# Kernel optimization log

Measured on AMD Instinct MI355X. Metric: run time of the kernel, lower is better.

The kernel has to match this reference:

```python
import jax, jax.numpy as jnp
import numpy as np

EPS = 1e-6                                   # VN leaky-relu denominator eps
BN_SCALE = np.float32(1.0 / np.sqrt(1.0 + 1e-5))  # eval-mode BatchNorm with default stats
NEG = 0.2                                    # negative_slope


def vn_lin(x, w):
    # x: [n, c, 3, ...]; w: [c, o] -> [n, o, 3, ...]
    return jnp.einsum('nc...,co->no...', x, w)


def vn_act(p, d):
    # Vector-Neuron leaky ReLU: project p off the half-space defined by direction d.
    dot = jnp.sum(p * d, axis=2, keepdims=True)
    dsq = jnp.sum(d * d, axis=2, keepdims=True)
    corr = p - (dot / (dsq + EPS)) * d
    return NEG * p + (1.0 - NEG) * jnp.where(dot >= 0, p, corr)


def score_net(x, w_vn, wd_vn, w_h1, w_h2, b_h2, temp=1.0):
    # CorrelationNet: VNLinearLeakyReLU(3 -> 2*ks) -> norm -> 1x1 convs -> softmax
    p = vn_lin(x, w_vn) * BN_SCALE           # [N, 2ks, 3, K] (VNBatchNorm ~ scalar in eval)
    d = vn_lin(x, wd_vn)
    s = vn_act(p, d)
    s = jnp.linalg.norm(s, axis=2)           # [N, 2ks, K]
    s = jax.nn.relu(jnp.einsum('nck,co->nok', s, w_h1) * BN_SCALE)  # conv1d k=1, BN, relu
    s = jnp.einsum('nck,co->nok', s, w_h2) + b_h2[None, :, None]     # last conv with bias
    return jax.nn.softmax(s / temp, axis=1)  # [N, ks, K]


def setup_inputs() -> dict:
    key = jax.random.key(0)
    k = [jax.random.fold_in(key, i) for i in range(13)]
    N, N2, K, KS, OUT = 16000, 20000, 16, 8, 64
    half = OUT // 2
    return {
        'q_pts': jax.random.normal(k[0], (N, 3), jnp.float32),
        's_pts': jax.random.normal(k[1], (N2, 3), jnp.float32),
        's_feats': jax.random.normal(k[2], (N2, 1, 3), jnp.float32),
        'neighbor_indices': jax.random.randint(k[3], (N, K), 0, N2),
        'wb': jax.random.normal(k[4], (3, KS * half), jnp.float32) * np.float32(np.sqrt(2.0 / 3.0)),
        'w_vn': jax.random.normal(k[5], (3, 2 * KS), jnp.float32) * 0.5,
        'wd_vn': jax.random.normal(k[6], (3, 2 * KS), jnp.float32) * 0.5,
        'w_h1': jax.random.normal(k[7], (2 * KS, KS), jnp.float32) * 0.25,
        'w_h2': jax.random.normal(k[8], (KS, KS), jnp.float32) * 0.35,
        'b_h2': jnp.zeros((KS,), jnp.float32),
        'wd_relu': jax.random.normal(k[9], (half, half), jnp.float32) * 0.18,
        'w_un': jax.random.normal(k[10], (half, OUT), jnp.float32) * 0.18,
        'wd_un': jax.random.normal(k[11], (half, OUT), jnp.float32) * 0.18,
    }


def reference(q_pts, s_pts, s_feats, neighbor_indices, wb, w_vn, wd_vn,
              w_h1, w_h2, b_h2, wd_relu, w_un, wd_un):
    N, K = neighbor_indices.shape
    KS = w_h2.shape[1]
    # neighbor gather + centering: [N, K, 3] -> [N, 1, 3, K]
    pts = s_pts[neighbor_indices] - q_pts[:, None]
    pts = jnp.transpose(pts, (0, 2, 1))[:, None]
    centers = jnp.broadcast_to(jnp.mean(pts, axis=-1, keepdims=True), pts.shape)
    cross = jnp.cross(pts, centers, axis=2)
    local = jnp.concatenate([pts, centers, cross], axis=1)   # [N, 3, 3, K]
    scores = score_net(local, w_vn, wd_vn, w_h1, w_h2, b_h2)  # [N, KS, K]
    # kernel-point correlation conv
    pro = jnp.einsum('ncdk,cf->nfdk', local, wb)              # [N, KS*half, 3, K]
    pro = pro.reshape(N, KS, -1, 3, K)
    pro = jnp.sum(pro * scores[:, :, None, None, :], axis=1)  # [N, half, 3, K]
    nrm = jnp.linalg.norm(pro, axis=2, keepdims=True)
    normed = pro / jnp.maximum(nrm, 1e-12)                    # F.normalize(p=2, dim=2)
    feats = jnp.mean(normed, axis=-1)                         # [N, half, 3]
    feats = vn_act(feats, vn_lin(feats, wd_relu))             # VNLeakyReLU
    out = vn_act(vn_lin(feats, w_un) * BN_SCALE, vn_lin(feats, wd_un))  # VNLinearLeakyReLU
    return out                                                # [N, out_dim, 3]
```

## Files before the change

### kernel.cpp

```cpp
#include <hip/hip_runtime.h>
#include <math.h>

#define VN_EPS   1e-6f
#define NEG      0.2f
#define POS      0.8f

typedef float v2f __attribute__((ext_vector_type(2)));
typedef float v4f __attribute__((ext_vector_type(4)));

template <int CTRL>
__device__ __forceinline__ float dpp_add(float v) {
    int s = __builtin_amdgcn_update_dpp(0, __float_as_int(v), CTRL, 0xf, 0xf, true);
    return v + __int_as_float(s);
}
__device__ __forceinline__ float row16_allsum(float v) {
    v = dpp_add<0x128>(v);
    v = dpp_add<0x124>(v);
    v = dpp_add<0x122>(v);
    v = dpp_add<0x121>(v);
    return v;
}
__device__ __forceinline__ float row16_sum15(float v) {
    v = dpp_add<0x118>(v);
    v = dpp_add<0x114>(v);
    v = dpp_add<0x112>(v);
    v = dpp_add<0x111>(v);
    return v;
}

__global__ __launch_bounds__(128) void areconv_kernel(
    const float* __restrict__ q_pts,
    const float* __restrict__ s_pts,
    const int*   __restrict__ nbr,
    const float* __restrict__ wb,
    const float* __restrict__ w_vn,
    const float* __restrict__ wd_vn,
    const float* __restrict__ w_h1,
    const float* __restrict__ w_h2,
    const float* __restrict__ b_h2,
    const float* __restrict__ wd_relu,
    const float* __restrict__ w_un,
    const float* __restrict__ wd_un,
    float* __restrict__ out,
    int N)
{
    const float BN_SCALE = 0.999994993f;

    __shared__ __align__(16) float featsA [8][3][36];
    __shared__ __align__(16) float feats2A[8][3][36];

    const int tid  = threadIdx.x;
    const int wv   = tid >> 6;
    const int lane = tid & 63;
    const int p    = lane >> 4;
    const int k    = lane & 15;
    const int bp   = wv * 4 + p;
    int n = blockIdx.x * 8 + bp;
    n = (n < N) ? n : (N - 1);

    const float qx = q_pts[n * 3 + 0];
    const float qy = q_pts[n * 3 + 1];
    const float qz = q_pts[n * 3 + 2];
    const int   id = nbr[n * 16 + k];
    const float px = s_pts[id * 3 + 0] - qx;
    const float py = s_pts[id * 3 + 1] - qy;
    const float pz = s_pts[id * 3 + 2] - qz;

    const float cx = row16_allsum(px) * 0.0625f;
    const float cy = row16_allsum(py) * 0.0625f;
    const float cz = row16_allsum(pz) * 0.0625f;

    const float rx = py * cz - pz * cy;
    const float ry = pz * cx - px * cz;
    const float rz = px * cy - py * cx;

    const float L[3][3] = {{px, py, pz}, {cx, cy, cz}, {rx, ry, rz}};

    v2f t01 = {0.f, 0.f}, t23 = t01, t45 = t01, t67 = t01;
#pragma unroll 1
    for (int o = 0; o < 16; ++o) {
        const float wv0 = w_vn[o],  wv1 = w_vn[16 + o],  wv2 = w_vn[32 + o];
        const float wd0 = wd_vn[o], wd1 = wd_vn[16 + o], wd2 = wd_vn[32 + o];
        float pv[3], dv[3];
        float dot = 0.f, dsq = 0.f;
#pragma unroll
        for (int d = 0; d < 3; ++d) {
            const float pp = BN_SCALE * (L[0][d] * wv0 + L[1][d] * wv1 + L[2][d] * wv2);
            const float dd = L[0][d] * wd0 + L[1][d] * wd1 + L[2][d] * wd2;
            pv[d] = pp; dv[d] = dd;
            dot += pp * dd;
            dsq += dd * dd;
        }
        const float f = dot * __builtin_amdgcn_rcpf(dsq + VN_EPS);
        float acc = 0.f;
#pragma unroll
        for (int d = 0; d < 3; ++d) {
            const float corr = pv[d] - f * dv[d];
            const float sel  = (dot >= 0.f) ? pv[d] : corr;
            const float a    = NEG * pv[d] + POS * sel;
            acc += a * a;
        }
        const float s = __builtin_amdgcn_sqrtf(acc);
        t01 += s * (*(const v2f*)&w_h1[o * 8 + 0]);
        t23 += s * (*(const v2f*)&w_h1[o * 8 + 2]);
        t45 += s * (*(const v2f*)&w_h1[o * 8 + 4]);
        t67 += s * (*(const v2f*)&w_h1[o * 8 + 6]);
    }
    float tt[8];
    tt[0] = fmaxf(t01[0] * BN_SCALE, 0.f);  tt[1] = fmaxf(t01[1] * BN_SCALE, 0.f);
    tt[2] = fmaxf(t23[0] * BN_SCALE, 0.f);  tt[3] = fmaxf(t23[1] * BN_SCALE, 0.f);
    tt[4] = fmaxf(t45[0] * BN_SCALE, 0.f);  tt[5] = fmaxf(t45[1] * BN_SCALE, 0.f);
    tt[6] = fmaxf(t67[0] * BN_SCALE, 0.f);  tt[7] = fmaxf(t67[1] * BN_SCALE, 0.f);

    float sc[8];
    float mx = -1e30f;
#pragma unroll
    for (int op = 0; op < 4; ++op) {
        v2f u = *(const v2f*)&b_h2[2 * op];
#pragma unroll
        for (int c = 0; c < 8; ++c)
            u += tt[c] * (*(const v2f*)&w_h2[c * 8 + 2 * op]);
        sc[2 * op + 0] = u[0];
        sc[2 * op + 1] = u[1];
        mx = fmaxf(mx, fmaxf(u[0], u[1]));
    }
    float se = 0.f;
#pragma unroll
    for (int o = 0; o < 8; ++o) { sc[o] = __expf(sc[o] - mx); se += sc[o]; }
    const float inv_se = __builtin_amdgcn_rcpf(se);
#pragma unroll
    for (int o = 0; o < 8; ++o) sc[o] *= inv_se;

#pragma unroll 1
    for (int grp = 0; grp < 8; ++grp) {
        const int hb = grp * 4;
        v4f W0 = sc[0] * (*(const v4f*)&wb[0 * 256 + hb]);
        v4f W1 = sc[0] * (*(const v4f*)&wb[1 * 256 + hb]);
        v4f W2 = sc[0] * (*(const v4f*)&wb[2 * 256 + hb]);
#pragma unroll
        for (int s = 1; s < 8; ++s) {
            const float sv = sc[s];
            W0 += sv * (*(const v4f*)&wb[0 * 256 + s * 32 + hb]);
            W1 += sv * (*(const v4f*)&wb[1 * 256 + s * 32 + hb]);
            W2 += sv * (*(const v4f*)&wb[2 * 256 + s * 32 + hb]);
        }
        v4f V0 = L[0][0] * W0 + L[1][0] * W1 + L[2][0] * W2;
        v4f V1 = L[0][1] * W0 + L[1][1] * W1 + L[2][1] * W2;
        v4f V2 = L[0][2] * W0 + L[1][2] * W1 + L[2][2] * W2;
        v4f vv = V0 * V0 + V1 * V1 + V2 * V2;
        v4f inn;
#pragma unroll
        for (int e = 0; e < 4; ++e)
            inn[e] = __builtin_amdgcn_rsqf(fmaxf(vv[e], 1e-24f)) * 0.0625f;
        V0 *= inn; V1 *= inn; V2 *= inn;
        v4f X0, X1, X2;
#pragma unroll
        for (int e = 0; e < 4; ++e) {
            X0[e] = row16_sum15(V0[e]);
            X1[e] = row16_sum15(V1[e]);
            X2[e] = row16_sum15(V2[e]);
        }
        if (k == 15) {
            *(v4f*)&featsA[bp][0][hb] = X0;
            *(v4f*)&featsA[bp][1][hb] = X1;
            *(v4f*)&featsA[bp][2][hb] = X2;
        }
    }

    {
        v2f D0 = {0.f, 0.f}, D1 = D0, D2 = D0;
#pragma unroll 1
        for (int grp = 0; grp < 8; ++grp) {
            const int hb = grp * 4;
            const v4f f0 = *(const v4f*)&featsA[bp][0][hb];
            const v4f f1 = *(const v4f*)&featsA[bp][1][hb];
            const v4f f2 = *(const v4f*)&featsA[bp][2][hb];
#pragma unroll
            for (int e = 0; e < 4; ++e) {
                const v2f w = *(const v2f*)&wd_relu[(hb + e) * 32 + 2 * k];
                D0 += f0[e] * w;
                D1 += f1[e] * w;
                D2 += f2[e] * w;
            }
        }
        v2f R0, R1, R2;
#pragma unroll
        for (int j = 0; j < 2; ++j) {
            const int o = 2 * k + j;
            const float p0 = featsA[bp][0][o];
            const float p1 = featsA[bp][1][o];
            const float p2 = featsA[bp][2][o];
            const float d0 = D0[j], d1 = D1[j], d2 = D2[j];
            const float dot = p0 * d0 + p1 * d1 + p2 * d2;
            const float dsq = d0 * d0 + d1 * d1 + d2 * d2;
            const float f   = dot * __builtin_amdgcn_rcpf(dsq + VN_EPS);
            const bool  pos = (dot >= 0.f);
            R0[j] = NEG * p0 + POS * (pos ? p0 : (p0 - f * d0));
            R1[j] = NEG * p1 + POS * (pos ? p1 : (p1 - f * d1));
            R2[j] = NEG * p2 + POS * (pos ? p2 : (p2 - f * d2));
        }
        *(v2f*)&feats2A[bp][0][2 * k] = R0;
        *(v2f*)&feats2A[bp][1][2 * k] = R1;
        *(v2f*)&feats2A[bp][2][2 * k] = R2;
    }

    {
        v4f AU0 = (v4f)0.f, AU1 = AU0, AU2 = AU0;
        v4f AV0 = AU0, AV1 = AU0, AV2 = AU0;
#pragma unroll 1
        for (int grp = 0; grp < 8; ++grp) {
            const int hb = grp * 4;
            const v4f f0 = *(const v4f*)&feats2A[bp][0][hb];
            const v4f f1 = *(const v4f*)&feats2A[bp][1][hb];
            const v4f f2 = *(const v4f*)&feats2A[bp][2][hb];
#pragma unroll
            for (int e = 0; e < 4; ++e) {
                const v4f wu = *(const v4f*)&w_un [(hb + e) * 64 + 4 * k];
                const v4f wd = *(const v4f*)&wd_un[(hb + e) * 64 + 4 * k];
                AU0 += f0[e] * wu; AU1 += f1[e] * wu; AU2 += f2[e] * wu;
                AV0 += f0[e] * wd; AV1 += f1[e] * wd; AV2 += f2[e] * wd;
            }
        }
        float O[12];
#pragma unroll
        for (int e = 0; e < 4; ++e) {
            const float u0 = AU0[e] * BN_SCALE;
            const float u1 = AU1[e] * BN_SCALE;
            const float u2 = AU2[e] * BN_SCALE;
            const float v0 = AV0[e], v1 = AV1[e], v2 = AV2[e];
            const float dot = u0 * v0 + u1 * v1 + u2 * v2;
            const float dsq = v0 * v0 + v1 * v1 + v2 * v2;
            const float f   = dot * __builtin_amdgcn_rcpf(dsq + VN_EPS);
            const bool  pos = (dot >= 0.f);
            O[3 * e + 0] = NEG * u0 + POS * (pos ? u0 : (u0 - f * v0));
            O[3 * e + 1] = NEG * u1 + POS * (pos ? u1 : (u1 - f * v1));
            O[3 * e + 2] = NEG * u2 + POS * (pos ? u2 : (u2 - f * v2));
        }
        float* dst = out + (long)n * 192 + 12 * k;
        *(v4f*)(dst + 0) = *(const v4f*)&O[0];
        *(v4f*)(dst + 4) = *(const v4f*)&O[4];
        *(v4f*)(dst + 8) = *(const v4f*)&O[8];
    }
}

extern "C" void kernel_launch(void* const* d_in, const int* in_sizes, int n_in,
                              void* d_out, int out_size, void* d_ws, size_t ws_size,
                              hipStream_t stream) {
    const float* q_pts   = (const float*)d_in[0];
    const float* s_pts   = (const float*)d_in[1];
    const int*   nbr     = (const int*)  d_in[3];
    const float* wb      = (const float*)d_in[4];
    const float* w_vn    = (const float*)d_in[5];
    const float* wd_vn   = (const float*)d_in[6];
    const float* w_h1    = (const float*)d_in[7];
    const float* w_h2    = (const float*)d_in[8];
    const float* b_h2    = (const float*)d_in[9];
    const float* wd_relu = (const float*)d_in[10];
    const float* w_un    = (const float*)d_in[11];
    const float* wd_un   = (const float*)d_in[12];
    float* out = (float*)d_out;

    const int N = in_sizes[0] / 3;
    const int blocks = (N + 7) / 8;
    areconv_kernel<<<blocks, 128, 0, stream>>>(
        q_pts, s_pts, nbr, wb, w_vn, wd_vn, w_h1, w_h2, b_h2,
        wd_relu, w_un, wd_un, out, N);
}
```

Baseline: 108.0 us.

## Split each point's channels across two lane groups and stage weights in LDS

Each query point now gets 32 lanes instead of 16. The two 16-lane halves split the score-net output channels, and a swizzle reduction combines their partial sums. They also split the projection-head and output channels, and the block handles 4 points instead of 8. The wb, w_vn, wd_vn and w_h1 weights are preloaded into shared memory per block, and a launch-bounds occupancy hint is added. This halves the serial per-lane work and doubles the thread count, but it duplicates the neighbor gather and the softmax/score computation in both halves and adds a per-block weight load plus a barrier.

```diff
diff --git a/kernel.cpp b/kernel.cpp
--- a/kernel.cpp
+++ b/kernel.cpp
@@ -27,8 +27,11 @@
     v = dpp_add<0x111>(v);
     return v;
 }
-
-__global__ __launch_bounds__(128) void areconv_kernel(
+__device__ __forceinline__ float swz_xor16(float v) {
+    return __int_as_float(__builtin_amdgcn_ds_swizzle(__float_as_int(v), 0x401F));
+}
+
+__global__ __launch_bounds__(128, 8) void areconv_kernel(
     const float* __restrict__ q_pts,
     const float* __restrict__ s_pts,
     const int*   __restrict__ nbr,
@@ -46,16 +49,27 @@
 {
     const float BN_SCALE = 0.999994993f;
 
-    __shared__ __align__(16) float featsA [8][3][36];
-    __shared__ __align__(16) float feats2A[8][3][36];
-
-    const int tid  = threadIdx.x;
+    __shared__ __align__(16) float featsA [4][3][36];
+    __shared__ __align__(16) float feats2A[4][3][36];
+    __shared__ __align__(16) float swb  [768];
+    __shared__ __align__(16) float swvn [48];
+    __shared__ __align__(16) float swdvn[48];
+    __shared__ __align__(16) float swh1 [128];
+
+    const int tid = threadIdx.x;
+    if (tid < 48) { swvn[tid] = w_vn[tid]; swdvn[tid] = wd_vn[tid]; }
+    swh1[tid] = w_h1[tid];
+#pragma unroll
+    for (int i = 0; i < 6; ++i) swb[tid + 128 * i] = wb[tid + 128 * i];
+    __syncthreads();
+
     const int wv   = tid >> 6;
     const int lane = tid & 63;
-    const int p    = lane >> 4;
+    const int p    = lane >> 5;
+    const int og   = (lane >> 4) & 1;
     const int k    = lane & 15;
-    const int bp   = wv * 4 + p;
-    int n = blockIdx.x * 8 + bp;
+    const int bp   = wv * 2 + p;
+    int n = blockIdx.x * 4 + bp;
     n = (n < N) ? n : (N - 1);
 
     const float qx = q_pts[n * 3 + 0];
@@ -78,9 +92,10 @@
 
     v2f t01 = {0.f, 0.f}, t23 = t01, t45 = t01, t67 = t01;
 #pragma unroll 1
-    for (int o = 0; o < 16; ++o) {
-        const float wv0 = w_vn[o],  wv1 = w_vn[16 + o],  wv2 = w_vn[32 + o];
-        const float wd0 = wd_vn[o], wd1 = wd_vn[16 + o], wd2 = wd_vn[32 + o];
+    for (int o8 = 0; o8 < 8; ++o8) {
+        const int o = og * 8 + o8;
+        const float wv0 = swvn[o],  wv1 = swvn[16 + o],  wv2 = swvn[32 + o];
+        const float wd0 = swdvn[o], wd1 = swdvn[16 + o], wd2 = swdvn[32 + o];
         float pv[3], dv[3];
         float dot = 0.f, dsq = 0.f;
 #pragma unroll
@@ -101,11 +116,16 @@
             acc += a * a;
         }
         const float s = __builtin_amdgcn_sqrtf(acc);
-        t01 += s * (*(const v2f*)&w_h1[o * 8 + 0]);
-        t23 += s * (*(const v2f*)&w_h1[o * 8 + 2]);
-        t45 += s * (*(const v2f*)&w_h1[o * 8 + 4]);
-        t67 += s * (*(const v2f*)&w_h1[o * 8 + 6]);
-    }
+        t01 += s * (*(const v2f*)&swh1[o * 8 + 0]);
+        t23 += s * (*(const v2f*)&swh1[o * 8 + 2]);
+        t45 += s * (*(const v2f*)&swh1[o * 8 + 4]);
+        t67 += s * (*(const v2f*)&swh1[o * 8 + 6]);
+    }
+    t01[0] += swz_xor16(t01[0]);  t01[1] += swz_xor16(t01[1]);
+    t23[0] += swz_xor16(t23[0]);  t23[1] += swz_xor16(t23[1]);
+    t45[0] += swz_xor16(t45[0]);  t45[1] += swz_xor16(t45[1]);
+    t67[0] += swz_xor16(t67[0]);  t67[1] += swz_xor16(t67[1]);
+
     float tt[8];
     tt[0] = fmaxf(t01[0] * BN_SCALE, 0.f);  tt[1] = fmaxf(t01[1] * BN_SCALE, 0.f);
     tt[2] = fmaxf(t23[0] * BN_SCALE, 0.f);  tt[3] = fmaxf(t23[1] * BN_SCALE, 0.f);
@@ -132,43 +152,40 @@
     for (int o = 0; o < 8; ++o) sc[o] *= inv_se;
 
 #pragma unroll 1
-    for (int grp = 0; grp < 8; ++grp) {
-        const int hb = grp * 4;
-        v4f W0 = sc[0] * (*(const v4f*)&wb[0 * 256 + hb]);
-        v4f W1 = sc[0] * (*(const v4f*)&wb[1 * 256 + hb]);
-        v4f W2 = sc[0] * (*(const v4f*)&wb[2 * 256 + hb]);
+    for (int gi = 0; gi < 4; ++gi) {
+        const int hb = og * 16 + gi * 4;
+        v4f W0 = sc[0] * (*(const v4f*)&swb[0 * 256 + hb]);
+        v4f W1 = sc[0] * (*(const v4f*)&swb[1 * 256 + hb]);
+        v4f W2 = sc[0] * (*(const v4f*)&swb[2 * 256 + hb]);
 #pragma unroll
         for (int s = 1; s < 8; ++s) {
             const float sv = sc[s];
-            W0 += sv * (*(const v4f*)&wb[0 * 256 + s * 32 + hb]);
-            W1 += sv * (*(const v4f*)&wb[1 * 256 + s * 32 + hb]);
-            W2 += sv * (*(const v4f*)&wb[2 * 256 + s * 32 + hb]);
+            W0 += sv * (*(const v4f*)&swb[0 * 256 + s * 32 + hb]);
+            W1 += sv * (*(const v4f*)&swb[1 * 256 + s * 32 + hb]);
+            W2 += sv * (*(const v4f*)&swb[2 * 256 + s * 32 + hb]);
         }
         v4f V0 = L[0][0] * W0 + L[1][0] * W1 + L[2][0] * W2;
         v4f V1 = L[0][1] * W0 + L[1][1] * W1 + L[2][1] * W2;
         v4f V2 = L[0][2] * W0 + L[1][2] * W1 + L[2][2] * W2;
-        v4f vv = V0 * V0 + V1 * V1 + V2 * V2;
-        v4f inn;
-#pragma unroll
-        for (int e = 0; e < 4; ++e)
-            inn[e] = __builtin_amdgcn_rsqf(fmaxf(vv[e], 1e-24f)) * 0.0625f;
-        V0 *= inn; V1 *= inn; V2 *= inn;
-        v4f X0, X1, X2;
+        const v4f vv = V0 * V0 + V1 * V1 + V2 * V2;
 #pragma unroll
         for (int e = 0; e < 4; ++e) {
-            X0[e] = row16_sum15(V0[e]);
-            X1[e] = row16_sum15(V1[e]);
-            X2[e] = row16_sum15(V2[e]);
+            const float inn = __builtin_amdgcn_rsqf(fmaxf(vv[e], 1e-24f)) * 0.0625f;
+            V0[e] = row16_sum15(V0[e] * inn);
+            V1[e] = row16_sum15(V1[e] * inn);
+            V2[e] = row16_sum15(V2[e] * inn);
         }
         if (k == 15) {
-            *(v4f*)&featsA[bp][0][hb] = X0;
-            *(v4f*)&featsA[bp][1][hb] = X1;
-            *(v4f*)&featsA[bp][2][hb] = X2;
-        }
-    }
+            *(v4f*)&featsA[bp][0][hb] = V0;
+            *(v4f*)&featsA[bp][1][hb] = V1;
+            *(v4f*)&featsA[bp][2][hb] = V2;
+        }
+    }
+
+    const int oo = og * 16 + k;
 
     {
-        v2f D0 = {0.f, 0.f}, D1 = D0, D2 = D0;
+        float D0 = 0.f, D1 = 0.f, D2 = 0.f;
 #pragma unroll 1
         for (int grp = 0; grp < 8; ++grp) {
             const int hb = grp * 4;
@@ -177,36 +194,27 @@
             const v4f f2 = *(const v4f*)&featsA[bp][2][hb];
 #pragma unroll
             for (int e = 0; e < 4; ++e) {
-                const v2f w = *(const v2f*)&wd_relu[(hb + e) * 32 + 2 * k];
+                const float w = wd_relu[(hb + e) * 32 + oo];
                 D0 += f0[e] * w;
                 D1 += f1[e] * w;
                 D2 += f2[e] * w;
             }
         }
-        v2f R0, R1, R2;
-#pragma unroll
-        for (int j = 0; j < 2; ++j) {
-            const int o = 2 * k + j;
-            const float p0 = featsA[bp][0][o];
-            const float p1 = featsA[bp][1][o];
-            const float p2 = featsA[bp][2][o];
-            const float d0 = D0[j], d1 = D1[j], d2 = D2[j];
-            const float dot = p0 * d0 + p1 * d1 + p2 * d2;
-            const float dsq = d0 * d0 + d1 * d1 + d2 * d2;
-            const float f   = dot * __builtin_amdgcn_rcpf(dsq + VN_EPS);
-            const bool  pos = (dot >= 0.f);
-            R0[j] = NEG * p0 + POS * (pos ? p0 : (p0 - f * d0));
-            R1[j] = NEG * p1 + POS * (pos ? p1 : (p1 - f * d1));
-            R2[j] = NEG * p2 + POS * (pos ? p2 : (p2 - f * d2));
-        }
-        *(v2f*)&feats2A[bp][0][2 * k] = R0;
-        *(v2f*)&feats2A[bp][1][2 * k] = R1;
-        *(v2f*)&feats2A[bp][2][2 * k] = R2;
+        const float p0 = featsA[bp][0][oo];
+        const float p1 = featsA[bp][1][oo];
+        const float p2 = featsA[bp][2][oo];
+        const float dot = p0 * D0 + p1 * D1 + p2 * D2;
+        const float dsq = D0 * D0 + D1 * D1 + D2 * D2;
+        const float f   = dot * __builtin_amdgcn_rcpf(dsq + VN_EPS);
+        const bool  pos = (dot >= 0.f);
+        feats2A[bp][0][oo] = NEG * p0 + POS * (pos ? p0 : (p0 - f * D0));
+        feats2A[bp][1][oo] = NEG * p1 + POS * (pos ? p1 : (p1 - f * D1));
+        feats2A[bp][2][oo] = NEG * p2 + POS * (pos ? p2 : (p2 - f * D2));
     }
 
     {
-        v4f AU0 = (v4f)0.f, AU1 = AU0, AU2 = AU0;
-        v4f AV0 = AU0, AV1 = AU0, AV2 = AU0;
+        v2f AU0 = {0.f, 0.f}, AU1 = AU0, AU2 = AU0;
+        v2f AV0 = AU0, AV1 = AU0, AV2 = AU0;
 #pragma unroll 1
         for (int grp = 0; grp < 8; ++grp) {
             const int hb = grp * 4;
@@ -215,31 +223,31 @@
             const v4f f2 = *(const v4f*)&feats2A[bp][2][hb];
 #pragma unroll
             for (int e = 0; e < 4; ++e) {
-                const v4f wu = *(const v4f*)&w_un [(hb + e) * 64 + 4 * k];
-                const v4f wd = *(const v4f*)&wd_un[(hb + e) * 64 + 4 * k];
+                const v2f wu = *(const v2f*)&w_un [(hb + e) * 64 + 2 * oo];
+                const v2f wd = *(const v2f*)&wd_un[(hb + e) * 64 + 2 * oo];
                 AU0 += f0[e] * wu; AU1 += f1[e] * wu; AU2 += f2[e] * wu;
                 AV0 += f0[e] * wd; AV1 += f1[e] * wd; AV2 += f2[e] * wd;
             }
         }
-        float O[12];
-#pragma unroll
-        for (int e = 0; e < 4; ++e) {
-            const float u0 = AU0[e] * BN_SCALE;
-            const float u1 = AU1[e] * BN_SCALE;
-            const float u2 = AU2[e] * BN_SCALE;
-            const float v0 = AV0[e], v1 = AV1[e], v2 = AV2[e];
+        float O[6];
+#pragma unroll
+        for (int j = 0; j < 2; ++j) {
+            const float u0 = AU0[j] * BN_SCALE;
+            const float u1 = AU1[j] * BN_SCALE;
+            const float u2 = AU2[j] * BN_SCALE;
+            const float v0 = AV0[j], v1 = AV1[j], v2 = AV2[j];
             const float dot = u0 * v0 + u1 * v1 + u2 * v2;
             const float dsq = v0 * v0 + v1 * v1 + v2 * v2;
             const float f   = dot * __builtin_amdgcn_rcpf(dsq + VN_EPS);
             const bool  pos = (dot >= 0.f);
-            O[3 * e + 0] = NEG * u0 + POS * (pos ? u0 : (u0 - f * v0));
-            O[3 * e + 1] = NEG * u1 + POS * (pos ? u1 : (u1 - f * v1));
-            O[3 * e + 2] = NEG * u2 + POS * (pos ? u2 : (u2 - f * v2));
-        }
-        float* dst = out + (long)n * 192 + 12 * k;
-        *(v4f*)(dst + 0) = *(const v4f*)&O[0];
-        *(v4f*)(dst + 4) = *(const v4f*)&O[4];
-        *(v4f*)(dst + 8) = *(const v4f*)&O[8];
+            O[3 * j + 0] = NEG * u0 + POS * (pos ? u0 : (u0 - f * v0));
+            O[3 * j + 1] = NEG * u1 + POS * (pos ? u1 : (u1 - f * v1));
+            O[3 * j + 2] = NEG * u2 + POS * (pos ? u2 : (u2 - f * v2));
+        }
+        float* dst = out + (long)n * 192 + 6 * oo;
+        *(v2f*)(dst + 0) = *(const v2f*)&O[0];
+        *(v2f*)(dst + 2) = *(const v2f*)&O[2];
+        *(v2f*)(dst + 4) = *(const v2f*)&O[4];
     }
 }
 
@@ -261,7 +269,7 @@
     float* out = (float*)d_out;
 
     const int N = in_sizes[0] / 3;
-    const int blocks = (N + 7) / 8;
+    const int blocks = (N + 3) / 4;
     areconv_kernel<<<blocks, 128, 0, stream>>>(
         q_pts, s_pts, nbr, wb, w_vn, wd_vn, w_h1, w_h2, b_h2,
         wd_relu, w_un, wd_un, out, N);
```

Result: slower. 155.9 us (+44.3%).
